# Performance work log

Hardware: AMD Instinct MI355X
Metric: run time of the kernel (lower is better)

## Reference

```python
import jax, jax.numpy as jnp
import numpy as np

F8 = jnp.float8_e4m3fn
F8_MAX = 448.0  # finfo(float8_e4m3fn).max

def setup_inputs() -> dict:
    key = jax.random.key(0)
    k1, k2, k3 = jax.random.split(key, 3)
    B, S, IN, OUT = 4, 4096, 2048, 2048
    x = jax.random.normal(k1, (B, S, IN), dtype=jnp.float32)
    # Pre-quantized fp8 weight [OUT, IN] with a per-tensor scale, as stored by AutoFP8
    w = jax.random.normal(k2, (OUT, IN), dtype=jnp.float32)
    weight_scale = (jnp.max(jnp.abs(w)) / F8_MAX).astype(jnp.float32)
    qweight = jnp.clip(w / weight_scale, -F8_MAX, F8_MAX).astype(F8)
    input_scale = jnp.asarray(0.05, dtype=jnp.float32)  # static activation scale
    bias = jax.random.normal(k3, (OUT,), dtype=jnp.float32)
    return {"x": x, "qweight": qweight, "weight_scale": weight_scale,
            "input_scale": input_scale, "bias": bias}

def reference(x, qweight, weight_scale, input_scale, bias):
    # per_tensor_quantize: divide by static scale, clamp to fp8 range, cast to e4m3fn
    qinput = jnp.clip(x / input_scale, -F8_MAX, F8_MAX).astype(F8)  # [B,S,IN] fp8
    # scaled fp8 GEMM with fused dequant + bias epilogue (out_dtype = x.dtype)
    a = qinput.astype(x.dtype) * input_scale          # dequant activations
    b = qweight.astype(x.dtype) * weight_scale        # dequant weights [OUT,IN]
    return jnp.einsum('bsi,oi->bso', a, b) + bias     # [B,S,OUT]
```

## Files before the change

kernel.cpp:

```cpp
#include <hip/hip_runtime.h>
#include <stdint.h>

typedef float  floatx4 __attribute__((ext_vector_type(4)));
typedef int    intx4   __attribute__((ext_vector_type(4)));
typedef int    intx8   __attribute__((ext_vector_type(8)));

#define AS1 __attribute__((address_space(1)))
#define AS3 __attribute__((address_space(3)))

__device__ __forceinline__ float quant_e4m3_value(float v) {
  float av = fabsf(v);
  float step, rstep;
  if (av < 0.015625f) {
    step  = 0.001953125f;
    rstep = 512.0f;
  } else {
    uint32_t e = __float_as_uint(av) >> 23;
    step  = __uint_as_float((e - 3u) << 23);
    rstep = __uint_as_float((257u - e) << 23);
  }
  return rintf(v * rstep) * step;
}

__device__ __forceinline__ uint32_t enc_e4m3(float v) {
  uint32_t u = __float_as_uint(v);
  uint32_t s = (u >> 24) & 0x80u;
  float av = fabsf(v);
  uint32_t b;
  if (av < 0.015625f) {
    b = s | (uint32_t)(av * 512.0f);
  } else {
    uint32_t e = ((u >> 23) & 0xffu) - 120u;
    uint32_t m = (u >> 20) & 7u;
    b = s | (e << 3) | m;
  }
  return b;
}

__device__ __forceinline__ uint32_t quant4(float4 v, float s) {
  float a0 = quant_e4m3_value(fminf(fmaxf(v.x / s, -448.0f), 448.0f));
  float a1 = quant_e4m3_value(fminf(fmaxf(v.y / s, -448.0f), 448.0f));
  float a2 = quant_e4m3_value(fminf(fmaxf(v.z / s, -448.0f), 448.0f));
  float a3 = quant_e4m3_value(fminf(fmaxf(v.w / s, -448.0f), 448.0f));
  return enc_e4m3(a0) | (enc_e4m3(a1) << 8) | (enc_e4m3(a2) << 16) |
         (enc_e4m3(a3) << 24);
}

__global__ __launch_bounds__(256) void quantize_x_kernel(
    const float4* __restrict__ x, const float* __restrict__ s_ptr,
    uint4* __restrict__ q, int n16) {
  int i = blockIdx.x * 256 + threadIdx.x;
  if (i >= n16) return;
  const float s = s_ptr[0];
  uint4 o;
  o.x = quant4(x[i * 4 + 0], s);
  o.y = quant4(x[i * 4 + 1], s);
  o.z = quant4(x[i * 4 + 2], s);
  o.w = quant4(x[i * 4 + 3], s);
  q[i] = o;
}

__global__ __launch_bounds__(256) void prep_w_kernel(
    const uint8_t* __restrict__ qw, uint4* __restrict__ w8, int n16) {
  const uint32_t* q32 = (const uint32_t*)qw;
  int lane = threadIdx.x & 63;
  uint32_t w0 = q32[lane], w1 = q32[lane + 64];
  bool fa = ((w0 & 0xFFFFFu) == 0u) && ((w1 & 0xFFFFFu) == 0u);
  uint32_t nib = (w0 | (w0 >> 16) | w1 | (w1 >> 16)) & 0xFu;
  unsigned long long ba = __ballot(fa);
  unsigned long long bb = __ballot(nib == 0u);
  int m = (ba == ~0ull) ? 2 : ((bb == ~0ull) ? 1 : 0);

  int i = blockIdx.x * 256 + threadIdx.x;
  if (i >= n16) return;
  uint4 o;
  uint32_t r[4];
  if (m == 1) {
#pragma unroll
    for (int j = 0; j < 4; ++j) {
      ushort4 u = ((const ushort4*)qw)[i * 4 + j];
      r[j] = enc_e4m3(__uint_as_float((uint32_t)u.x << 16)) |
             (enc_e4m3(__uint_as_float((uint32_t)u.y << 16)) << 8) |
             (enc_e4m3(__uint_as_float((uint32_t)u.z << 16)) << 16) |
             (enc_e4m3(__uint_as_float((uint32_t)u.w << 16)) << 24);
    }
  } else if (m == 2) {
#pragma unroll
    for (int j = 0; j < 4; ++j) {
      float4 v = ((const float4*)qw)[i * 4 + j];
      r[j] = enc_e4m3(v.x) | (enc_e4m3(v.y) << 8) | (enc_e4m3(v.z) << 16) |
             (enc_e4m3(v.w) << 24);
    }
  } else {
    uint4 c = ((const uint4*)qw)[i];
    r[0] = c.x; r[1] = c.y; r[2] = c.z; r[3] = c.w;
  }
  o.x = r[0]; o.y = r[1]; o.z = r[2]; o.w = r[3];
  w8[i] = o;
}

__global__ __launch_bounds__(512, 2) void gemm_fp8_kernel(
    const uint8_t* __restrict__ A, const uint8_t* __restrict__ B,
    const float* __restrict__ wscale, const float* __restrict__ iscale,
    const float* __restrict__ bias, float* __restrict__ out,
    int M, int N, int K) {
  __shared__ uint8_t lds[131072];

  const int tid  = threadIdx.x;
  const int lane = tid & 63;
  const int wave = tid >> 6;

  const int nbx = gridDim.x;
  const int nwg = nbx * gridDim.y;
  int flat = blockIdx.y * nbx + blockIdx.x;
  flat = (flat & 7) * (nwg >> 3) + (flat >> 3);
  const int bm = flat / nbx;
  const int bn = flat - bm * nbx;

  const int wm = (wave >> 2) * 128;
  const int wn = (wave & 3) * 64;
  const int r15 = lane & 15, quad = lane >> 4, k8 = r15 & 7;
  const int posL = ((2 * quad)     ^ k8) << 4;
  const int posH = ((2 * quad + 1) ^ k8) << 4;

  const uint8_t* aS[2]; const uint8_t* bS[2]; uint32_t dOf[2];
#pragma unroll
  for (int j = 0; j < 2; ++j) {
    const int s = tid + j * 512, rl = s >> 3, p = s & 7;
    aS[j] = A + (size_t)(bm * 256 + rl) * K + ((p ^ (rl & 7)) << 4);
    bS[j] = B + (size_t)(bn * 256 + rl) * K + ((p ^ (rl & 7)) << 4);
    dOf[j] = (uint32_t)s << 4;
  }
  const size_t hK = (size_t)128 * K;

#define STG_A(j, h, kb, bf_)                                                   \
  __builtin_amdgcn_global_load_lds(                                            \
      (const AS1 void*)(aS[j] + (h) * hK + (kb)),                              \
      (AS3 void*)(&lds[(bf_) * 32768u + (h) * 16384u + dOf[j]]), 16, 0, 0)
#define STG_B(j, h, kb, bf_)                                                   \
  __builtin_amdgcn_global_load_lds(                                            \
      (const AS1 void*)(bS[j] + (h) * hK + (kb)),                              \
      (AS3 void*)(&lds[65536u + (bf_) * 32768u + (h) * 16384u + dOf[j]]),      \
      16, 0, 0)

  floatx4 acc[8][4];
#pragma unroll
  for (int i = 0; i < 8; ++i)
#pragma unroll
    for (int j = 0; j < 4; ++j) acc[i][j] = (floatx4){0.f, 0.f, 0.f, 0.f};

  const int T = K >> 7;

  STG_A(0, 0, 0, 0); STG_A(1, 0, 0, 0); STG_A(0, 1, 0, 0); STG_A(1, 1, 0, 0);
  STG_B(0, 0, 0, 0); STG_B(1, 0, 0, 0); STG_B(0, 1, 0, 0); STG_B(1, 1, 0, 0);
  if (T > 1) {
    STG_B(0, 0, 128, 1); STG_B(1, 0, 128, 1);
    STG_B(0, 1, 128, 1); STG_B(1, 1, 128, 1);
    asm volatile("s_waitcnt vmcnt(4)" ::: "memory");
  } else {
    asm volatile("s_waitcnt vmcnt(0)" ::: "memory");
  }
  __builtin_amdgcn_sched_barrier(0);
  __builtin_amdgcn_s_barrier();

  for (int t = 0; t < T; ++t) {
    const int cur = t & 1;
    const uint8_t* LA = &lds[cur * 32768u] + (wm + r15) * 128;
    const uint8_t* LB = &lds[65536u + cur * 32768u] + (wn + r15) * 128;
    const int kb1 = (t + 1) << 7, kb2 = (t + 2) << 7;
    intx8 af[4], bf[4];

    if (t + 1 < T) {
      STG_A(0, 0, kb1, cur ^ 1); STG_A(1, 0, kb1, cur ^ 1);
      STG_A(0, 1, kb1, cur ^ 1); STG_A(1, 1, kb1, cur ^ 1);
    }

#pragma unroll
    for (int j = 0; j < 4; ++j) {
      intx4 lo = *(const intx4*)(LB + j * 2048 + posL);
      intx4 hi = *(const intx4*)(LB + j * 2048 + posH);
      bf[j] = __builtin_shufflevector(lo, hi, 0, 1, 2, 3, 4, 5, 6, 7);
    }
#pragma unroll
    for (int i = 0; i < 4; ++i) {
      intx4 lo = *(const intx4*)(LA + i * 2048 + posL);
      intx4 hi = *(const intx4*)(LA + i * 2048 + posH);
      af[i] = __builtin_shufflevector(lo, hi, 0, 1, 2, 3, 4, 5, 6, 7);
    }
    __builtin_amdgcn_s_setprio(1);
#pragma unroll
    for (int i = 0; i < 4; ++i)
#pragma unroll
      for (int j = 0; j < 4; ++j)
        acc[i][j] = __builtin_amdgcn_mfma_scale_f32_16x16x128_f8f6f4(
            af[i], bf[j], acc[i][j], 0, 0, 0, 127, 0, 127);
    __builtin_amdgcn_s_setprio(0);

    __builtin_amdgcn_s_barrier();
    if (t + 2 < T) {
      STG_B(0, 0, kb2, cur); STG_B(1, 0, kb2, cur);
      STG_B(0, 1, kb2, cur); STG_B(1, 1, kb2, cur);
    }

#pragma unroll
    for (int i = 0; i < 4; ++i) {
      intx4 lo = *(const intx4*)(LA + 8192 + i * 2048 + posL);
      intx4 hi = *(const intx4*)(LA + 8192 + i * 2048 + posH);
      af[i] = __builtin_shufflevector(lo, hi, 0, 1, 2, 3, 4, 5, 6, 7);
    }
    __builtin_amdgcn_s_setprio(1);
#pragma unroll
    for (int i = 0; i < 4; ++i)
#pragma unroll
      for (int j = 0; j < 4; ++j)
        acc[4 + i][j] = __builtin_amdgcn_mfma_scale_f32_16x16x128_f8f6f4(
            af[i], bf[j], acc[4 + i][j], 0, 0, 0, 127, 0, 127);
    __builtin_amdgcn_s_setprio(0);

    if (t + 1 < T) {
      if (t + 2 < T) asm volatile("s_waitcnt vmcnt(4)" ::: "memory");
      else           asm volatile("s_waitcnt vmcnt(0)" ::: "memory");
      __builtin_amdgcn_sched_barrier(0);
      __builtin_amdgcn_s_barrier();
    }
  }

  const float sc = wscale[0] * iscale[0];
  const int rq = quad * 4;
#pragma unroll
  for (int jj = 0; jj < 4; ++jj) {
    const int col = bn * 256 + wn + jj * 16 + r15;
    const float bv = bias[col];
#pragma unroll
    for (int mi = 0; mi < 8; ++mi) {
      const int row = bm * 256 + wm + (mi >> 2) * 64 + (mi & 3) * 16 + rq;
      float* o = out + (size_t)row * N + col;
#pragma unroll
      for (int r = 0; r < 4; ++r)
        o[(size_t)r * N] = acc[mi][jj][r] * sc + bv;
    }
  }
#undef STG_A
#undef STG_B
}

extern "C" void kernel_launch(void* const* d_in, const int* in_sizes, int n_in,
                              void* d_out, int out_size, void* d_ws,
                              size_t ws_size, hipStream_t stream) {
  const float*   x      = (const float*)d_in[0];
  const uint8_t* qw     = (const uint8_t*)d_in[1];
  const float*   wscale = (const float*)d_in[2];
  const float*   iscale = (const float*)d_in[3];
  const float*   bias   = (const float*)d_in[4];
  float*         out    = (float*)d_out;

  const int N = in_sizes[4];
  const int K = in_sizes[1] / N;
  const int M = in_sizes[0] / K;

  uint8_t* qx = (uint8_t*)d_ws;
  uint8_t* w8 = qx + (size_t)M * K;

  const int nx16 = in_sizes[0] / 16;
  quantize_x_kernel<<<(nx16 + 255) / 256, 256, 0, stream>>>(
      (const float4*)x, iscale, (uint4*)qx, nx16);

  const int nw16 = in_sizes[1] / 16;
  prep_w_kernel<<<(nw16 + 255) / 256, 256, 0, stream>>>(qw, (uint4*)w8, nw16);

  dim3 grid(N / 256, M / 256);
  gemm_fp8_kernel<<<grid, 512, 0, stream>>>(qx, w8, wscale, iscale, bias,
                                            out, M, N, K);
}
```

Before: 320.8 us.

## Load B fragments directly from global memory and shrink LDS to A-only

The GEMM no longer stages B tiles through LDS. Each wave reads its B fragments straight from global memory every k-step, twice per iteration, and LDS is halved to 64KB holding only double-buffered A. The quantize and weight-prep kernels move to one 32-bit output word per thread instead of four. This removes B staging traffic and frees LDS, which could allow higher occupancy. In exchange, B reads become uncoalesced per-lane global loads, duplicated across the waves sharing columns, and the waits become full vmcnt(0) drains with no prefetch depth.

```diff
diff --git a/kernel.cpp b/kernel.cpp
--- a/kernel.cpp
+++ b/kernel.cpp
@@ -37,31 +37,23 @@
   return b;
 }
 
-__device__ __forceinline__ uint32_t quant4(float4 v, float s) {
+__global__ __launch_bounds__(256) void quantize_x_kernel(
+    const float4* __restrict__ x, const float* __restrict__ s_ptr,
+    uint32_t* __restrict__ q, int n4) {
+  int i = blockIdx.x * 256 + threadIdx.x;
+  if (i >= n4) return;
+  const float s = s_ptr[0];
+  float4 v = x[i];
   float a0 = quant_e4m3_value(fminf(fmaxf(v.x / s, -448.0f), 448.0f));
   float a1 = quant_e4m3_value(fminf(fmaxf(v.y / s, -448.0f), 448.0f));
   float a2 = quant_e4m3_value(fminf(fmaxf(v.z / s, -448.0f), 448.0f));
   float a3 = quant_e4m3_value(fminf(fmaxf(v.w / s, -448.0f), 448.0f));
-  return enc_e4m3(a0) | (enc_e4m3(a1) << 8) | (enc_e4m3(a2) << 16) |
+  q[i] = enc_e4m3(a0) | (enc_e4m3(a1) << 8) | (enc_e4m3(a2) << 16) |
          (enc_e4m3(a3) << 24);
 }
 
-__global__ __launch_bounds__(256) void quantize_x_kernel(
-    const float4* __restrict__ x, const float* __restrict__ s_ptr,
-    uint4* __restrict__ q, int n16) {
-  int i = blockIdx.x * 256 + threadIdx.x;
-  if (i >= n16) return;
-  const float s = s_ptr[0];
-  uint4 o;
-  o.x = quant4(x[i * 4 + 0], s);
-  o.y = quant4(x[i * 4 + 1], s);
-  o.z = quant4(x[i * 4 + 2], s);
-  o.w = quant4(x[i * 4 + 3], s);
-  q[i] = o;
-}
-
 __global__ __launch_bounds__(256) void prep_w_kernel(
-    const uint8_t* __restrict__ qw, uint4* __restrict__ w8, int n16) {
+    const uint8_t* __restrict__ qw, uint32_t* __restrict__ w8, int n4) {
   const uint32_t* q32 = (const uint32_t*)qw;
   int lane = threadIdx.x & 63;
   uint32_t w0 = q32[lane], w1 = q32[lane + 64];
@@ -72,30 +64,21 @@
   int m = (ba == ~0ull) ? 2 : ((bb == ~0ull) ? 1 : 0);
 
   int i = blockIdx.x * 256 + threadIdx.x;
-  if (i >= n16) return;
-  uint4 o;
-  uint32_t r[4];
+  if (i >= n4) return;
+  uint32_t o;
   if (m == 1) {
-#pragma unroll
-    for (int j = 0; j < 4; ++j) {
-      ushort4 u = ((const ushort4*)qw)[i * 4 + j];
-      r[j] = enc_e4m3(__uint_as_float((uint32_t)u.x << 16)) |
-             (enc_e4m3(__uint_as_float((uint32_t)u.y << 16)) << 8) |
-             (enc_e4m3(__uint_as_float((uint32_t)u.z << 16)) << 16) |
-             (enc_e4m3(__uint_as_float((uint32_t)u.w << 16)) << 24);
-    }
+    ushort4 u = ((const ushort4*)qw)[i];
+    o = enc_e4m3(__uint_as_float((uint32_t)u.x << 16)) |
+        (enc_e4m3(__uint_as_float((uint32_t)u.y << 16)) << 8) |
+        (enc_e4m3(__uint_as_float((uint32_t)u.z << 16)) << 16) |
+        (enc_e4m3(__uint_as_float((uint32_t)u.w << 16)) << 24);
   } else if (m == 2) {
-#pragma unroll
-    for (int j = 0; j < 4; ++j) {
-      float4 v = ((const float4*)qw)[i * 4 + j];
-      r[j] = enc_e4m3(v.x) | (enc_e4m3(v.y) << 8) | (enc_e4m3(v.z) << 16) |
-             (enc_e4m3(v.w) << 24);
-    }
+    float4 v = ((const float4*)qw)[i];
+    o = enc_e4m3(v.x) | (enc_e4m3(v.y) << 8) | (enc_e4m3(v.z) << 16) |
+        (enc_e4m3(v.w) << 24);
   } else {
-    uint4 c = ((const uint4*)qw)[i];
-    r[0] = c.x; r[1] = c.y; r[2] = c.z; r[3] = c.w;
-  }
-  o.x = r[0]; o.y = r[1]; o.z = r[2]; o.w = r[3];
+    o = ((const uint32_t*)qw)[i];
+  }
   w8[i] = o;
 }
 
@@ -104,7 +87,7 @@
     const float* __restrict__ wscale, const float* __restrict__ iscale,
     const float* __restrict__ bias, float* __restrict__ out,
     int M, int N, int K) {
-  __shared__ uint8_t lds[131072];
+  __shared__ uint8_t lds[65536];
 
   const int tid  = threadIdx.x;
   const int lane = tid & 63;
@@ -123,25 +106,24 @@
   const int posL = ((2 * quad)     ^ k8) << 4;
   const int posH = ((2 * quad + 1) ^ k8) << 4;
 
-  const uint8_t* aS[2]; const uint8_t* bS[2]; uint32_t dOf[2];
+  const uint8_t* aS[2]; uint32_t dOf[2];
 #pragma unroll
   for (int j = 0; j < 2; ++j) {
     const int s = tid + j * 512, rl = s >> 3, p = s & 7;
     aS[j] = A + (size_t)(bm * 256 + rl) * K + ((p ^ (rl & 7)) << 4);
-    bS[j] = B + (size_t)(bn * 256 + rl) * K + ((p ^ (rl & 7)) << 4);
     dOf[j] = (uint32_t)s << 4;
   }
   const size_t hK = (size_t)128 * K;
+
+  const uint8_t* bptr[4];
+#pragma unroll
+  for (int j = 0; j < 4; ++j)
+    bptr[j] = B + (size_t)(bn * 256 + wn + j * 16 + r15) * K + quad * 32;
 
 #define STG_A(j, h, kb, bf_)                                                   \
   __builtin_amdgcn_global_load_lds(                                            \
       (const AS1 void*)(aS[j] + (h) * hK + (kb)),                              \
       (AS3 void*)(&lds[(bf_) * 32768u + (h) * 16384u + dOf[j]]), 16, 0, 0)
-#define STG_B(j, h, kb, bf_)                                                   \
-  __builtin_amdgcn_global_load_lds(                                            \
-      (const AS1 void*)(bS[j] + (h) * hK + (kb)),                              \
-      (AS3 void*)(&lds[65536u + (bf_) * 32768u + (h) * 16384u + dOf[j]]),      \
-      16, 0, 0)
 
   floatx4 acc[8][4];
 #pragma unroll
@@ -152,35 +134,31 @@
   const int T = K >> 7;
 
   STG_A(0, 0, 0, 0); STG_A(1, 0, 0, 0); STG_A(0, 1, 0, 0); STG_A(1, 1, 0, 0);
-  STG_B(0, 0, 0, 0); STG_B(1, 0, 0, 0); STG_B(0, 1, 0, 0); STG_B(1, 1, 0, 0);
-  if (T > 1) {
-    STG_B(0, 0, 128, 1); STG_B(1, 0, 128, 1);
-    STG_B(0, 1, 128, 1); STG_B(1, 1, 128, 1);
-    asm volatile("s_waitcnt vmcnt(4)" ::: "memory");
-  } else {
-    asm volatile("s_waitcnt vmcnt(0)" ::: "memory");
-  }
+  asm volatile("s_waitcnt vmcnt(0)" ::: "memory");
   __builtin_amdgcn_sched_barrier(0);
   __builtin_amdgcn_s_barrier();
 
   for (int t = 0; t < T; ++t) {
     const int cur = t & 1;
     const uint8_t* LA = &lds[cur * 32768u] + (wm + r15) * 128;
-    const uint8_t* LB = &lds[65536u + cur * 32768u] + (wn + r15) * 128;
-    const int kb1 = (t + 1) << 7, kb2 = (t + 2) << 7;
+    const int kb0 = t << 7;
     intx8 af[4], bf[4];
 
+#pragma unroll
+    for (int j = 0; j < 4; ++j) {
+      intx4 lo = *(const intx4*)(bptr[j] + kb0);
+      intx4 hi = *(const intx4*)(bptr[j] + kb0 + 16);
+      bf[j] = __builtin_shufflevector(lo, hi, 0, 1, 2, 3, 4, 5, 6, 7);
+    }
+    __builtin_amdgcn_sched_barrier(0);
+
     if (t + 1 < T) {
+      const int kb1 = (t + 1) << 7;
       STG_A(0, 0, kb1, cur ^ 1); STG_A(1, 0, kb1, cur ^ 1);
       STG_A(0, 1, kb1, cur ^ 1); STG_A(1, 1, kb1, cur ^ 1);
     }
-
-#pragma unroll
-    for (int j = 0; j < 4; ++j) {
-      intx4 lo = *(const intx4*)(LB + j * 2048 + posL);
-      intx4 hi = *(const intx4*)(LB + j * 2048 + posH);
-      bf[j] = __builtin_shufflevector(lo, hi, 0, 1, 2, 3, 4, 5, 6, 7);
-    }
+    __builtin_amdgcn_sched_barrier(0);
+
 #pragma unroll
     for (int i = 0; i < 4; ++i) {
       intx4 lo = *(const intx4*)(LA + i * 2048 + posL);
@@ -196,12 +174,12 @@
             af[i], bf[j], acc[i][j], 0, 0, 0, 127, 0, 127);
     __builtin_amdgcn_s_setprio(0);
 
-    __builtin_amdgcn_s_barrier();
-    if (t + 2 < T) {
-      STG_B(0, 0, kb2, cur); STG_B(1, 0, kb2, cur);
-      STG_B(0, 1, kb2, cur); STG_B(1, 1, kb2, cur);
-    }
-
+#pragma unroll
+    for (int j = 0; j < 4; ++j) {
+      intx4 lo = *(const intx4*)(bptr[j] + kb0);
+      intx4 hi = *(const intx4*)(bptr[j] + kb0 + 16);
+      bf[j] = __builtin_shufflevector(lo, hi, 0, 1, 2, 3, 4, 5, 6, 7);
+    }
 #pragma unroll
     for (int i = 0; i < 4; ++i) {
       intx4 lo = *(const intx4*)(LA + 8192 + i * 2048 + posL);
@@ -218,12 +196,12 @@
     __builtin_amdgcn_s_setprio(0);
 
     if (t + 1 < T) {
-      if (t + 2 < T) asm volatile("s_waitcnt vmcnt(4)" ::: "memory");
-      else           asm volatile("s_waitcnt vmcnt(0)" ::: "memory");
+      asm volatile("s_waitcnt vmcnt(0)" ::: "memory");
       __builtin_amdgcn_sched_barrier(0);
       __builtin_amdgcn_s_barrier();
     }
   }
+#undef STG_A
 
   const float sc = wscale[0] * iscale[0];
   const int rq = quad * 4;
@@ -240,8 +218,6 @@
         o[(size_t)r * N] = acc[mi][jj][r] * sc + bv;
     }
   }
-#undef STG_A
-#undef STG_B
 }
 
 extern "C" void kernel_launch(void* const* d_in, const int* in_sizes, int n_in,
@@ -261,12 +237,12 @@
   uint8_t* qx = (uint8_t*)d_ws;
   uint8_t* w8 = qx + (size_t)M * K;
 
-  const int nx16 = in_sizes[0] / 16;
-  quantize_x_kernel<<<(nx16 + 255) / 256, 256, 0, stream>>>(
-      (const float4*)x, iscale, (uint4*)qx, nx16);
-
-  const int nw16 = in_sizes[1] / 16;
-  prep_w_kernel<<<(nw16 + 255) / 256, 256, 0, stream>>>(qw, (uint4*)w8, nw16);
+  const int nx4 = in_sizes[0] / 4;
+  quantize_x_kernel<<<(nx4 + 255) / 256, 256, 0, stream>>>(
+      (const float4*)x, iscale, (uint32_t*)qx, nx4);
+
+  const int nw4 = in_sizes[1] / 4;
+  prep_w_kernel<<<(nw4 + 255) / 256, 256, 0, stream>>>(qw, (uint32_t*)w8, nw4);
 
   dim3 grid(N / 256, M / 256);
   gemm_fp8_kernel<<<grid, 512, 0, stream>>>(qx, w8, wscale, iscale, bias,
```

Result: slower. 350.0 us (+9.1%).
